# Optimization experiments

Measured on AMD Instinct MI355X. Metric: run time of the kernel, lower is better.

## Reference

```python
import jax, jax.numpy as jnp
import numpy as np

NODE_CARDS = [119, 5, 12, 12, 10, 6, 6, 2, 2]
EDGE_CARDS = [5, 6, 2]
HIDDEN = 256
LAYERS = 5
N = 60000
E = 180000
G = 2048  # num graphs (fixed num_segments)
BN_EPS = 1e-5

_NODE_OFFS = np.concatenate([[0], np.cumsum(NODE_CARDS[:-1])]).astype(np.int32)
_EDGE_OFFS = np.concatenate([[0], np.cumsum(EDGE_CARDS[:-1])]).astype(np.int32)
_NODE_MAX = np.asarray(NODE_CARDS, np.int32) - 1
_EDGE_MAX = np.asarray(EDGE_CARDS, np.int32) - 1


def _cat_sum(x, table, maxs, offs):
    # x: [N, F] int; table: [sum(cards), H] -> [N, H]
    idx = jnp.clip(x, 0, maxs[None, :]) + offs[None, :]
    return table[idx].sum(axis=1)


def setup_inputs() -> dict:
    key = jax.random.key(0)
    ks = jax.random.split(key, 32)
    w = 0.0625  # ~ xavier for 256

    def nrm(k, shape, s=w):
        return jax.random.normal(k, shape, dtype=jnp.float32) * s

    inp = {
        'x': jax.random.randint(ks[0], (N, len(NODE_CARDS)), 0, 119, dtype=jnp.int32),
        'edge_index': jax.random.randint(ks[1], (2, E), 0, N, dtype=jnp.int32),
        'edge_attr': jax.random.randint(ks[2], (E, len(EDGE_CARDS)), 0, 6, dtype=jnp.int32),
        'batch': jnp.sort(jax.random.randint(ks[3], (N,), 0, G, dtype=jnp.int32)),
        # embeddings
        'node_emb': nrm(ks[4], (int(sum(NODE_CARDS)), HIDDEN), 0.1),
        'edge_emb': nrm(ks[5], (int(sum(EDGE_CARDS)), HIDDEN), 0.1),
        'vn_emb': nrm(ks[6], (1, HIDDEN), 0.1),
        # GINE conv: eps + 2-layer MLP per layer (stacked)
        'eps': jnp.zeros((LAYERS,), jnp.float32),
        'W1': nrm(ks[7], (LAYERS, HIDDEN, HIDDEN)),
        'b1': jnp.zeros((LAYERS, HIDDEN), jnp.float32),
        'W2': nrm(ks[8], (LAYERS, HIDDEN, HIDDEN)),
        'b2': jnp.zeros((LAYERS, HIDDEN), jnp.float32),
        # BatchNorm (eval mode: running stats)
        'bn_gamma': jnp.ones((LAYERS, HIDDEN), jnp.float32),
        'bn_beta': jnp.zeros((LAYERS, HIDDEN), jnp.float32),
        'bn_mean': nrm(ks[9], (LAYERS, HIDDEN), 0.02),
        'bn_var': jnp.ones((LAYERS, HIDDEN), jnp.float32),
        # virtual-node MLP per layer
        'vW1': nrm(ks[10], (LAYERS, HIDDEN, HIDDEN)),
        'vb1': jnp.zeros((LAYERS, HIDDEN), jnp.float32),
        'vW2': nrm(ks[11], (LAYERS, HIDDEN, HIDDEN)),
        'vb2': jnp.zeros((LAYERS, HIDDEN), jnp.float32),
        # head MLP (2 layers: hidden->hidden->1)
        'hW1': nrm(ks[12], (HIDDEN, HIDDEN)),
        'hb1': jnp.zeros((HIDDEN,), jnp.float32),
        'hW2': nrm(ks[13], (HIDDEN, 1)),
        'hb2': jnp.zeros((1,), jnp.float32),
    }
    return inp


def reference(x, edge_index, edge_attr, batch,
              node_emb, edge_emb, vn_emb, eps,
              W1, b1, W2, b2,
              bn_gamma, bn_beta, bn_mean, bn_var,
              vW1, vb1, vW2, vb2,
              hW1, hb1, hW2, hb2):
    node_maxs = jnp.asarray(_NODE_MAX)
    node_offs = jnp.asarray(_NODE_OFFS)
    edge_maxs = jnp.asarray(_EDGE_MAX)
    edge_offs = jnp.asarray(_EDGE_OFFS)

    h = _cat_sum(x, node_emb, node_maxs, node_offs)          # [N, H]
    ea = _cat_sum(edge_attr, edge_emb, edge_maxs, edge_offs)  # [E, H]
    src, dst = edge_index[0], edge_index[1]

    vn = jnp.broadcast_to(vn_emb[0], (G, HIDDEN))  # [G, H]

    def mean_pool(h_):
        s = jax.ops.segment_sum(h_, batch, num_segments=G)
        cnt = jax.ops.segment_sum(jnp.ones((h_.shape[0], 1), h_.dtype), batch, num_segments=G)
        return s / jnp.maximum(cnt, 1.0)

    for l in range(LAYERS):
        h = h + vn[batch]
        # GINEConv: msg = relu(x_src + edge_attr); agg scatter-add onto dst
        msg = jax.nn.relu(h[src] + ea)                        # [E, H]
        agg = jax.ops.segment_sum(msg, dst, num_segments=N)   # [N, H]
        z = (1.0 + eps[l]) * h + agg
        z = jax.nn.relu(z @ W1[l] + b1[l]) @ W2[l] + b2[l]
        # BatchNorm1d (eval, running stats)
        z = (z - bn_mean[l]) * (bn_gamma[l] / jnp.sqrt(bn_var[l] + BN_EPS)) + bn_beta[l]
        h = jax.nn.relu(z)
        # virtual-node update
        g = mean_pool(h)
        vn = vn + (jax.nn.relu(g @ vW1[l] + vb1[l]) @ vW2[l] + vb2[l])

    g = mean_pool(h)                                          # [G, H]
    logits = (jax.nn.relu(g @ hW1 + hb1) @ hW2 + hb2).reshape(-1)  # [G]
    return logits
```

## Files before the change

kernel.cpp:

```cpp
#include <hip/hip_runtime.h>

#define NN 60000
#define NE 180000
#define NG 2048
#define NL 5
#define CAP 32

typedef unsigned short u16;
typedef unsigned int u32;
typedef __bf16 bf16x8 __attribute__((ext_vector_type(8)));
typedef float f32x4 __attribute__((ext_vector_type(4)));

__device__ __forceinline__ u16 f2bf(float f) {
    u32 u = __builtin_bit_cast(u32, f);
    u += 0x7FFFu + ((u >> 16) & 1u);
    return (u16)(u >> 16);
}
__device__ __forceinline__ float bf2f(u16 s) {
    return __builtin_bit_cast(float, (u32)s << 16);
}
__device__ __forceinline__ float bflo(u32 w) {
    return __builtin_bit_cast(float, w << 16);
}
__device__ __forceinline__ float bfhi(u32 w) {
    return __builtin_bit_cast(float, w & 0xFFFF0000u);
}
__device__ __forceinline__ u32 pack2bf(float lo, float hi) {
    return (u32)f2bf(lo) | ((u32)f2bf(hi) << 16);
}
__device__ __forceinline__ void gload_lds16(const void* g, void* l) {
    __builtin_amdgcn_global_load_lds(
        (const __attribute__((address_space(1))) unsigned int*)g,
        (__attribute__((address_space(3))) unsigned int*)l, 16, 0, 0);
}
__device__ __forceinline__ int swz(int row, int col) {
    return (row << 9) + ((((col >> 3) ^ (row & 7))) << 4) + ((col & 7) << 1);
}
__device__ __forceinline__ int bswz(int row) {
    return (row & 3) ^ ((row >> 2) & 3);
}

__constant__ int NODE_OFF[9]  = {0, 119, 124, 136, 148, 158, 164, 170, 172};
__constant__ int NODE_MAXC[9] = {118, 4, 11, 11, 9, 5, 5, 1, 1};

__global__ __launch_bounds__(256) void k_prep_weights(
    const float* __restrict__ W1, const float* __restrict__ W2,
    const float* __restrict__ vW1, const float* __restrict__ vW2,
    const float* __restrict__ hW1, u16* __restrict__ Wt)
{
    int mat = blockIdx.x >> 8;
    int n = blockIdx.x & 255;
    int k = threadIdx.x;
    const float* src;
    if (mat < 5)       src = W1 + (size_t)mat * 65536;
    else if (mat < 10) src = W2 + (size_t)(mat - 5) * 65536;
    else if (mat < 15) src = vW1 + (size_t)(mat - 10) * 65536;
    else if (mat < 20) src = vW2 + (size_t)(mat - 15) * 65536;
    else               src = hW1;
    Wt[(size_t)mat * 65536 + n * 256 + k] = f2bf(src[k * 256 + n]);
}

__global__ __launch_bounds__(256) void k_misc(
    const float* __restrict__ eemb, const int* __restrict__ batch,
    const float* __restrict__ vn_emb,
    u16* __restrict__ comb, int* __restrict__ starts,
    float* __restrict__ vn, u16* __restrict__ vnbf, float* __restrict__ gsum)
{
    int b = blockIdx.x;
    if (b < 2048) {
        int i = b * 256 + threadIdx.x;
        float v = vn_emb[i & 255];
        vn[i] = v;
        vnbf[i] = f2bf(v);
        gsum[i] = 0.f;
    } else if (b < 2108) {
        int r = b - 2048, c = threadIdx.x;
        int a0 = r / 12, a1 = (r % 12) / 2, a2 = r & 1;
        comb[r * 256 + c] = f2bf(eemb[a0 * 256 + c] + eemb[(5 + a1) * 256 + c] +
                                 eemb[(11 + a2) * 256 + c]);
    } else {
        int g = (b - 2108) * 256 + threadIdx.x;
        if (g > NG) return;
        int lo = 0, hi = NN;
        while (lo < hi) {
            int mid = (lo + hi) >> 1;
            if (batch[mid] < g) lo = mid + 1; else hi = mid;
        }
        starts[g] = lo;
    }
}

__global__ __launch_bounds__(256) void k_embed(const int* __restrict__ x,
                                               const float* __restrict__ node_emb,
                                               u16* __restrict__ hbf,
                                               int* __restrict__ deg)
{
    int i = blockIdx.x * 4 + (threadIdx.x >> 6);
    if (i >= NN) return;
    if ((threadIdx.x & 63) == 0) deg[i] = 0;
    int c = (threadIdx.x & 63) * 4;
    float4 s = make_float4(0.f, 0.f, 0.f, 0.f);
#pragma unroll
    for (int f = 0; f < 9; ++f) {
        int xv = x[i * 9 + f];
        xv = xv < 0 ? 0 : (xv > NODE_MAXC[f] ? NODE_MAXC[f] : xv);
        const float4 t = *(const float4*)&node_emb[(size_t)(NODE_OFF[f] + xv) * 256 + c];
        s.x += t.x; s.y += t.y; s.z += t.z; s.w += t.w;
    }
    ushort4 o;
    o.x = f2bf(s.x); o.y = f2bf(s.y); o.z = f2bf(s.z); o.w = f2bf(s.w);
    *(ushort4*)&hbf[(size_t)i * 256 + c] = o;
}

__global__ __launch_bounds__(256) void k_bucket(
    const int* __restrict__ src, const int* __restrict__ dst,
    const int* __restrict__ eattr, int* __restrict__ deg, u32* __restrict__ slots)
{
    int e = blockIdx.x * 256 + threadIdx.x;
    if (e >= NE) return;
    int a0 = eattr[e * 3 + 0]; a0 = a0 < 0 ? 0 : (a0 > 4 ? 4 : a0);
    int a1 = eattr[e * 3 + 1]; a1 = a1 < 0 ? 0 : (a1 > 5 ? 5 : a1);
    int a2 = eattr[e * 3 + 2]; a2 = a2 < 0 ? 0 : (a2 > 1 ? 1 : a2);
    u32 code = (u32)(a0 * 12 + a1 * 2 + a2);
    int d = dst[e];
    int p = atomicAdd(&deg[d], 1);
    if (p < CAP) slots[(size_t)d * CAP + p] = (u32)src[e] | (code << 17);
}

__global__ __launch_bounds__(256) void k_agg(
    const u16* __restrict__ hbf, const u16* __restrict__ vnbf,
    const int* __restrict__ batch, const u32* __restrict__ slots,
    const int* __restrict__ deg, const u16* __restrict__ comb,
    u16* __restrict__ Abf, const float* __restrict__ epsp)
{
    const int wid = threadIdx.x >> 6, lane = threadIdx.x & 63;
    const int half = lane >> 5, l32 = lane & 31;
    const int d = blockIdx.x * 8 + wid * 2 + half;
    const int c = l32 * 8;
    int nd = deg[d];
    nd = nd > CAP ? CAP : nd;

    const u32* sl = slots + (size_t)d * CAP;
    u32 sv_l = (l32 < nd) ? sl[l32] : 0u;
    int b_l = (l32 < nd) ? batch[sv_l & 0x1FFFFu] : 0;

    float acc[8] = {0.f, 0.f, 0.f, 0.f, 0.f, 0.f, 0.f, 0.f};
    for (int p = 0; p < nd; ++p) {
        int srcl = (lane & 32) | p;
        u32 sv = (u32)__shfl((int)sv_l, srcl);
        int b  = __shfl(b_l, srcl);
        int s  = (int)(sv & 0x1FFFFu);
        int code = (int)(sv >> 17);
        const uint4 hv = *(const uint4*)&hbf[(size_t)s * 256 + c];
        const uint4 vv = *(const uint4*)&vnbf[(size_t)b * 256 + c];
        const uint4 tv = *(const uint4*)&comb[(size_t)code * 256 + c];
        const u32* hw = (const u32*)&hv;
        const u32* vw = (const u32*)&vv;
        const u32* tw = (const u32*)&tv;
#pragma unroll
        for (int e = 0; e < 4; ++e) {
            acc[e * 2 + 0] += fmaxf(bflo(hw[e]) + bflo(vw[e]) + bflo(tw[e]), 0.f);
            acc[e * 2 + 1] += fmaxf(bfhi(hw[e]) + bfhi(vw[e]) + bfhi(tw[e]), 0.f);
        }
    }

    int bd = batch[d];
    float ep = 1.0f + *epsp;
    const uint4 hd = *(const uint4*)&hbf[(size_t)d * 256 + c];
    const uint4 vd = *(const uint4*)&vnbf[(size_t)bd * 256 + c];
    const u32* hw = (const u32*)&hd;
    const u32* vw = (const u32*)&vd;
    uint4 o;
    u32* op = (u32*)&o;
#pragma unroll
    for (int e = 0; e < 4; ++e) {
        float lo = (bflo(hw[e]) + bflo(vw[e])) * ep + acc[e * 2 + 0];
        float hi = (bfhi(hw[e]) + bfhi(vw[e])) * ep + acc[e * 2 + 1];
        op[e] = pack2bf(lo, hi);
    }
    *(uint4*)&Abf[(size_t)d * 256 + c] = o;
}

__device__ __forceinline__ void stageW32(const u16* __restrict__ W, u16* Bp,
                                         int k0, int tid, int wid)
{
#pragma unroll
    for (int i = 0; i < 2; ++i) {
        int slot = i * 512 + tid;
        int row = slot >> 2, cch = slot & 3;
        int g = cch ^ bswz(row);
        gload_lds16((const char*)W + (size_t)row * 512 + (size_t)k0 * 2 + (g << 4),
                    (char*)Bp + ((i * 512 + wid * 64) << 4));
    }
}

__device__ __forceinline__ void gemmPhase32(const u16* Tl, const u16* Bp,
                                            f32x4 (&acc)[2][4], int p,
                                            int wm, int wn, int cl, int rg)
{
    bf16x8 af[2], bfr[4];
    int ch = p * 4 + rg;
#pragma unroll
    for (int t = 0; t < 2; ++t) {
        int ar = wm + t * 16 + cl;
        af[t] = __builtin_bit_cast(bf16x8,
            *(const uint4*)((const char*)Tl + (ar << 9) + ((ch ^ (ar & 7)) << 4)));
    }
#pragma unroll
    for (int u = 0; u < 4; ++u) {
        int br = wn + u * 16 + cl;
        bfr[u] = __builtin_bit_cast(bf16x8,
            *(const uint4*)((const char*)Bp + (br << 6) + ((rg ^ bswz(br)) << 4)));
    }
#pragma unroll
    for (int t = 0; t < 2; ++t)
#pragma unroll
        for (int u = 0; u < 4; ++u)
            acc[t][u] = __builtin_amdgcn_mfma_f32_16x16x32_bf16(af[t], bfr[u], acc[t][u], 0, 0, 0);
}

__device__ __forceinline__ void writeT(u16* Tl, const f32x4 (&acc)[2][4],
                                       const float* __restrict__ b1,
                                       int wm, int wn, int lane)
{
    const int cl = lane & 15, rg = lane >> 4;
#pragma unroll
    for (int j = 0; j < 4; ++j) {
        int col = wn + j * 16 + cl;
        float bv = b1[col];
#pragma unroll
        for (int i = 0; i < 2; ++i)
#pragma unroll
            for (int r = 0; r < 4; ++r) {
                int row = wm + i * 16 + rg * 4 + r;
                float v = fmaxf(acc[i][j][r] + bv, 0.f);
                *(u16*)((char*)Tl + swz(row, col)) = f2bf(v);
            }
    }
}

__global__ __launch_bounds__(512) void k_mlpP2(
    const u16* __restrict__ Abf, u16* __restrict__ hnxt,
    const int* __restrict__ batch,
    const u16* __restrict__ W1t, const u16* __restrict__ W2t,
    const float* __restrict__ b1, const float* __restrict__ b2,
    const float* __restrict__ bng, const float* __restrict__ bnb,
    const float* __restrict__ bnm, const float* __restrict__ bnv,
    float* __restrict__ gsum)
{
    __shared__ __align__(16) u16 Tl[64 * 256];
    __shared__ __align__(16) u16 Bl[2][256 * 32];
    __shared__ int batchLds[64];
    const int m0 = blockIdx.x * 64;
    const int tid = threadIdx.x, lane = tid & 63, wid = tid >> 6;
    const int wm = (wid >> 2) * 32, wn = (wid & 3) * 64;
    const int cl = lane & 15, rg = lane >> 4;

    if (tid < 64) batchLds[tid] = (m0 + tid < NN) ? batch[m0 + tid] : -1;

#pragma unroll
    for (int i = 0; i < 4; ++i) {
        int slot = i * 512 + tid;
        int row = slot >> 5, cch = slot & 31;
        int g = cch ^ (row & 7);
        gload_lds16((const char*)Abf + (size_t)(m0 + row) * 512 + (g << 4),
                    (char*)Tl + ((i * 512 + wid * 64) << 4));
    }
    stageW32(W1t, Bl[0], 0, tid, wid);
    __syncthreads();

    f32x4 acc1[2][4] = {};
#pragma unroll
    for (int p = 0; p < 8; ++p) {
        if (p < 7) stageW32(W1t, Bl[(p + 1) & 1], (p + 1) * 32, tid, wid);
        else       stageW32(W2t, Bl[0], 0, tid, wid);
        gemmPhase32(Tl, Bl[p & 1], acc1, p, wm, wn, cl, rg);
        __syncthreads();
    }

    writeT(Tl, acc1, b1, wm, wn, lane);
    __syncthreads();

    f32x4 acc2[2][4] = {};
#pragma unroll
    for (int p = 0; p < 8; ++p) {
        if (p < 7) stageW32(W2t, Bl[(p + 1) & 1], (p + 1) * 32, tid, wid);
        gemmPhase32(Tl, Bl[p & 1], acc2, p, wm, wn, cl, rg);
        __syncthreads();
    }

#pragma unroll
    for (int j = 0; j < 4; ++j) {
        int gn = wn + j * 16 + cl;
        float bv = b2[gn];
        float sc = bng[gn] * rsqrtf(bnv[gn] + 1e-5f);
        float sh = bnb[gn] - bnm[gn] * sc;
        float s = 0.f;
        int gcur = -1;
#pragma unroll
        for (int i = 0; i < 2; ++i) {
#pragma unroll
            for (int r = 0; r < 4; ++r) {
                int row = wm + i * 16 + rg * 4 + r;
                int g = batchLds[row];
                float v = acc2[i][j][r] + bv;
                u16 hb = f2bf(fmaxf(v * sc + sh, 0.f));
                if (g >= 0) hnxt[(size_t)(m0 + row) * 256 + gn] = hb;
                if (g != gcur) {
                    if (gcur >= 0) atomicAdd(&gsum[(size_t)gcur * 256 + gn], s);
                    gcur = g; s = 0.f;
                }
                if (g >= 0) s += bf2f(hb);
            }
        }
        if (gcur >= 0) atomicAdd(&gsum[(size_t)gcur * 256 + gn], s);
    }
}

__device__ __forceinline__ void stageW(const u16* __restrict__ W, u16* Bl,
                                       int k0, int tid, int wid)
{
#pragma unroll
    for (int i = 0; i < 4; ++i) {
        int slot = i * 512 + tid;
        int row = slot >> 3, cch = slot & 7;
        int g = cch ^ (row & 7);
        gload_lds16((const char*)W + (size_t)row * 512 + (size_t)k0 * 2 + (g << 4),
                    (char*)Bl + ((i * 512 + wid * 64) << 4));
    }
}

__device__ __forceinline__ void gemm64(const u16* Tl, u16* Bl, const u16* __restrict__ W,
                                       f32x4 (&acc)[2][4], int wm, int wn,
                                       int lane, int tid, int wid)
{
    const int cl = lane & 15;
    for (int k0 = 0; k0 < 256; k0 += 64) {
        __syncthreads();
        stageW(W, Bl, k0, tid, wid);
        __syncthreads();
#pragma unroll
        for (int kw = 0; kw < 2; ++kw) {
            int q = kw * 4 + (lane >> 4);
            int qt = (k0 >> 3) + q;
            bf16x8 af[2], bfr[4];
#pragma unroll
            for (int t = 0; t < 2; ++t) {
                int ar = wm + t * 16 + cl;
                af[t] = __builtin_bit_cast(bf16x8,
                    *(const uint4*)((const char*)Tl + (ar << 9) + ((qt ^ (ar & 7)) << 4)));
            }
#pragma unroll
            for (int t = 0; t < 4; ++t) {
                int br = wn + t * 16 + cl;
                bfr[t] = __builtin_bit_cast(bf16x8,
                    *(const uint4*)((const char*)Bl + (br << 7) + ((q ^ (br & 7)) << 4)));
            }
#pragma unroll
            for (int i = 0; i < 2; ++i)
#pragma unroll
                for (int j = 0; j < 4; ++j)
                    acc[i][j] = __builtin_amdgcn_mfma_f32_16x16x32_bf16(af[i], bfr[j], acc[i][j], 0, 0, 0);
        }
    }
}

__global__ __launch_bounds__(512) void k_vnmlp(
    float* __restrict__ gsum, const int* __restrict__ starts,
    const u16* __restrict__ W1t, const u16* __restrict__ W2t,
    const float* __restrict__ b1, const float* __restrict__ b2,
    float* __restrict__ vn, u16* __restrict__ vnbf)
{
    __shared__ __align__(16) u16 Bl[256 * 64];
    __shared__ __align__(16) u16 Tl[64 * 256];
    const int m0 = blockIdx.x * 64;
    const int tid = threadIdx.x, lane = tid & 63, wid = tid >> 6;
    const int wm = (wid >> 2) * 32, wn = (wid & 3) * 64;
    const int cl = lane & 15, rg = lane >> 4;

    {
        const int c = lane * 4;
#pragma unroll
        for (int n = 0; n < 8; ++n) {
            int row = wid * 8 + n;
            int g = m0 + row;
            float4 sv = *(const float4*)&gsum[(size_t)g * 256 + c];
            *(float4*)&gsum[(size_t)g * 256 + c] = make_float4(0.f, 0.f, 0.f, 0.f);
            float cnt = (float)(starts[g + 1] - starts[g]);
            float inv = 1.0f / fmaxf(cnt, 1.0f);
            ushort4 o;
            o.x = f2bf(sv.x * inv); o.y = f2bf(sv.y * inv);
            o.z = f2bf(sv.z * inv); o.w = f2bf(sv.w * inv);
            *(ushort4*)((char*)Tl + swz(row, c)) = o;
        }
    }
    __syncthreads();

    f32x4 acc1[2][4] = {};
    gemm64(Tl, Bl, W1t, acc1, wm, wn, lane, tid, wid);
    __syncthreads();
    writeT(Tl, acc1, b1, wm, wn, lane);

    f32x4 acc2[2][4] = {};
    gemm64(Tl, Bl, W2t, acc2, wm, wn, lane, tid, wid);

#pragma unroll
    for (int j = 0; j < 4; ++j) {
        int gn = wn + j * 16 + cl;
        float bv = b2[gn];
#pragma unroll
        for (int i = 0; i < 2; ++i) {
#pragma unroll
            for (int r = 0; r < 4; ++r) {
                int gm = m0 + wm + i * 16 + rg * 4 + r;
                size_t idx = (size_t)gm * 256 + gn;
                float nv = vn[idx] + acc2[i][j][r] + bv;
                vn[idx] = nv;
                vnbf[idx] = f2bf(nv);
            }
        }
    }
}

__global__ __launch_bounds__(512) void k_headf(
    const float* __restrict__ gsum, const int* __restrict__ starts,
    const u16* __restrict__ W1t, const float* __restrict__ b1,
    const float* __restrict__ hW2, const float* __restrict__ hb2,
    float* __restrict__ out)
{
    __shared__ __align__(16) u16 Bl[256 * 64];
    __shared__ __align__(16) u16 Tl[64 * 256];
    const int m0 = blockIdx.x * 64;
    const int tid = threadIdx.x, lane = tid & 63, wid = tid >> 6;
    const int wm = (wid >> 2) * 32, wn = (wid & 3) * 64;

    {
        const int c = lane * 4;
#pragma unroll
        for (int n = 0; n < 8; ++n) {
            int row = wid * 8 + n;
            int g = m0 + row;
            float4 sv = *(const float4*)&gsum[(size_t)g * 256 + c];
            float cnt = (float)(starts[g + 1] - starts[g]);
            float inv = 1.0f / fmaxf(cnt, 1.0f);
            ushort4 o;
            o.x = f2bf(sv.x * inv); o.y = f2bf(sv.y * inv);
            o.z = f2bf(sv.z * inv); o.w = f2bf(sv.w * inv);
            *(ushort4*)((char*)Tl + swz(row, c)) = o;
        }
    }
    __syncthreads();

    f32x4 acc1[2][4] = {};
    gemm64(Tl, Bl, W1t, acc1, wm, wn, lane, tid, wid);
    __syncthreads();
    writeT(Tl, acc1, b1, wm, wn, lane);
    __syncthreads();

    int row = tid >> 3, oct = tid & 7;
    float s = 0.f;
#pragma unroll
    for (int c = 0; c < 32; ++c) {
        int col = oct * 32 + c;
        s += bf2f(*(const u16*)((const char*)Tl + swz(row, col))) * hW2[col];
    }
    s += __shfl_down(s, 4);
    s += __shfl_down(s, 2);
    s += __shfl_down(s, 1);
    if (oct == 0) out[m0 + row] = s + hb2[0];
}

extern "C" void kernel_launch(void* const* d_in, const int* in_sizes, int n_in,
                              void* d_out, int out_size, void* d_ws, size_t ws_size,
                              hipStream_t stream)
{
    const int*   x        = (const int*)d_in[0];
    const int*   ei       = (const int*)d_in[1];
    const int*   eattr    = (const int*)d_in[2];
    const int*   batch    = (const int*)d_in[3];
    const float* node_emb = (const float*)d_in[4];
    const float* edge_emb = (const float*)d_in[5];
    const float* vn_emb   = (const float*)d_in[6];
    const float* eps      = (const float*)d_in[7];
    const float* W1       = (const float*)d_in[8];
    const float* b1       = (const float*)d_in[9];
    const float* W2       = (const float*)d_in[10];
    const float* b2       = (const float*)d_in[11];
    const float* bng      = (const float*)d_in[12];
    const float* bnb      = (const float*)d_in[13];
    const float* bnm      = (const float*)d_in[14];
    const float* bnv      = (const float*)d_in[15];
    const float* vW1      = (const float*)d_in[16];
    const float* vb1      = (const float*)d_in[17];
    const float* vW2      = (const float*)d_in[18];
    const float* vb2      = (const float*)d_in[19];
    const float* hW1      = (const float*)d_in[20];
    const float* hb1      = (const float*)d_in[21];
    const float* hW2      = (const float*)d_in[22];
    const float* hb2      = (const float*)d_in[23];
    float* out = (float*)d_out;

    char* ws = (char*)d_ws;
    size_t off = 0;
    auto alloc = [&](size_t b) {
        char* p = ws + off;
        off = (off + b + 255) & ~(size_t)255;
        return p;
    };
    u16*   hbf0 = (u16*)alloc((size_t)NN * 256 * 2);
    u16*   hbf1 = (u16*)alloc((size_t)NN * 256 * 2);
    u16*   Abf  = (u16*)alloc((size_t)NN * 256 * 2 + 65536);
    float* vn   = (float*)alloc((size_t)NG * 256 * 4);
    u16*   vnbf = (u16*)alloc((size_t)NG * 256 * 2);
    float* gsum = (float*)alloc((size_t)NG * 256 * 4);
    u16*   Wt   = (u16*)alloc((size_t)21 * 65536 * 2);
    int*   starts = (int*)alloc((size_t)(NG + 1) * 4);
    u16*   comb = (u16*)alloc((size_t)60 * 256 * 2);
    int*   deg  = (int*)alloc((size_t)NN * 4);
    u32*   slots = (u32*)alloc((size_t)NN * CAP * 4);

    const int* srcI = ei;
    const int* dstI = ei + NE;

    k_prep_weights<<<21 * 256, 256, 0, stream>>>(W1, W2, vW1, vW2, hW1, Wt);
    k_misc<<<2117, 256, 0, stream>>>(edge_emb, batch, vn_emb, comb, starts, vn, vnbf, gsum);
    k_embed<<<NN / 4, 256, 0, stream>>>(x, node_emb, hbf0, deg);
    k_bucket<<<(NE + 255) / 256, 256, 0, stream>>>(srcI, dstI, eattr, deg, slots);

    const int GBIG = (NN + 63) / 64;
    const int GSM  = NG / 64;

    u16* hcur = hbf0;
    u16* hnxt = hbf1;
    for (int l = 0; l < NL; ++l) {
        k_agg<<<NN / 8, 256, 0, stream>>>(hcur, vnbf, batch, slots, deg, comb, Abf, eps + l);
        k_mlpP2<<<GBIG, 512, 0, stream>>>(Abf, hnxt, batch,
                                          Wt + (size_t)(0 + l) * 65536,
                                          Wt + (size_t)(5 + l) * 65536,
                                          b1 + l * 256, b2 + l * 256,
                                          bng + l * 256, bnb + l * 256,
                                          bnm + l * 256, bnv + l * 256,
                                          gsum);
        if (l < NL - 1) {
            k_vnmlp<<<GSM, 512, 0, stream>>>(gsum, starts,
                                             Wt + (size_t)(10 + l) * 65536,
                                             Wt + (size_t)(15 + l) * 65536,
                                             vb1 + l * 256, vb2 + l * 256,
                                             vn, vnbf);
        }
        u16* t = hcur; hcur = hnxt; hnxt = t;
    }
    k_headf<<<GSM, 512, 0, stream>>>(gsum, starts, Wt + (size_t)20 * 65536,
                                     hb1, hW2, hb2, out);
}
```

Measured before the change: 546.2 us.

## Tile weight transpose via LDS, remap agg blocks per XCD, use single-buffer 64-wide GEMM

The weight-prep kernel now transposes 64x64 tiles through shared memory with vectorized loads and stores, replacing strided per-element reads. The aggregation kernel remaps block IDs so that each XCD handles a contiguous range of destination nodes, which is meant to improve L2 locality. The node MLP kernel drops the double-buffered 32-wide K staging and reuses the existing single-buffer 64-wide gemm64 path. That gives fewer barriers per K step but no overlap between staging the weights and the MFMA work.

New measurement: 542.1 us. About the same (-0.8%).

```diff
diff --git a/kernel.cpp b/kernel.cpp
--- a/kernel.cpp
+++ b/kernel.cpp
@@ -36,9 +36,6 @@
 __device__ __forceinline__ int swz(int row, int col) {
     return (row << 9) + ((((col >> 3) ^ (row & 7))) << 4) + ((col & 7) << 1);
 }
-__device__ __forceinline__ int bswz(int row) {
-    return (row & 3) ^ ((row >> 2) & 3);
-}
 
 __constant__ int NODE_OFF[9]  = {0, 119, 124, 136, 148, 158, 164, 170, 172};
 __constant__ int NODE_MAXC[9] = {118, 4, 11, 11, 9, 5, 5, 1, 1};
@@ -48,16 +45,36 @@
     const float* __restrict__ vW1, const float* __restrict__ vW2,
     const float* __restrict__ hW1, u16* __restrict__ Wt)
 {
-    int mat = blockIdx.x >> 8;
-    int n = blockIdx.x & 255;
-    int k = threadIdx.x;
+    __shared__ float lt[64][65];
+    int mat = blockIdx.x >> 4;
+    int tile = blockIdx.x & 15;
+    int tr = (tile >> 2) * 64;
+    int tc = (tile & 3) * 64;
     const float* src;
     if (mat < 5)       src = W1 + (size_t)mat * 65536;
     else if (mat < 10) src = W2 + (size_t)(mat - 5) * 65536;
     else if (mat < 15) src = vW1 + (size_t)(mat - 10) * 65536;
     else if (mat < 20) src = vW2 + (size_t)(mat - 15) * 65536;
     else               src = hW1;
-    Wt[(size_t)mat * 65536 + n * 256 + k] = f2bf(src[k * 256 + n]);
+    int tid = threadIdx.x;
+#pragma unroll
+    for (int r = 0; r < 4; ++r) {
+        int k = (tid >> 4) + r * 16;
+        int c = (tid & 15) * 4;
+        float4 v = *(const float4*)&src[(size_t)(tr + k) * 256 + tc + c];
+        lt[k][c + 0] = v.x; lt[k][c + 1] = v.y;
+        lt[k][c + 2] = v.z; lt[k][c + 3] = v.w;
+    }
+    __syncthreads();
+#pragma unroll
+    for (int r = 0; r < 4; ++r) {
+        int n = (tid >> 4) + r * 16;
+        int k = (tid & 15) * 4;
+        ushort4 o;
+        o.x = f2bf(lt[k + 0][n]); o.y = f2bf(lt[k + 1][n]);
+        o.z = f2bf(lt[k + 2][n]); o.w = f2bf(lt[k + 3][n]);
+        *(ushort4*)&Wt[(size_t)mat * 65536 + (size_t)(tc + n) * 256 + tr + k] = o;
+    }
 }
 
 __global__ __launch_bounds__(256) void k_misc(
@@ -133,9 +150,14 @@
     const int* __restrict__ deg, const u16* __restrict__ comb,
     u16* __restrict__ Abf, const float* __restrict__ epsp)
 {
+    const int nwg = NN / 8;
+    const int q = nwg / 8, r = nwg % 8;
+    int xcd = blockIdx.x % 8, idx = blockIdx.x / 8;
+    int bid = (xcd < r ? xcd * (q + 1) : r * (q + 1) + (xcd - r) * q) + idx;
+
     const int wid = threadIdx.x >> 6, lane = threadIdx.x & 63;
     const int half = lane >> 5, l32 = lane & 31;
-    const int d = blockIdx.x * 8 + wid * 2 + half;
+    const int d = bid * 8 + wid * 2 + half;
     const int c = l32 * 8;
     int nd = deg[d];
     nd = nd > CAP ? CAP : nd;
@@ -181,42 +203,52 @@
     *(uint4*)&Abf[(size_t)d * 256 + c] = o;
 }
 
-__device__ __forceinline__ void stageW32(const u16* __restrict__ W, u16* Bp,
-                                         int k0, int tid, int wid)
-{
-#pragma unroll
-    for (int i = 0; i < 2; ++i) {
+__device__ __forceinline__ void stageW(const u16* __restrict__ W, u16* Bl,
+                                       int k0, int tid, int wid)
+{
+#pragma unroll
+    for (int i = 0; i < 4; ++i) {
         int slot = i * 512 + tid;
-        int row = slot >> 2, cch = slot & 3;
-        int g = cch ^ bswz(row);
+        int row = slot >> 3, cch = slot & 7;
+        int g = cch ^ (row & 7);
         gload_lds16((const char*)W + (size_t)row * 512 + (size_t)k0 * 2 + (g << 4),
-                    (char*)Bp + ((i * 512 + wid * 64) << 4));
-    }
-}
-
-__device__ __forceinline__ void gemmPhase32(const u16* Tl, const u16* Bp,
-                                            f32x4 (&acc)[2][4], int p,
-                                            int wm, int wn, int cl, int rg)
-{
-    bf16x8 af[2], bfr[4];
-    int ch = p * 4 + rg;
-#pragma unroll
-    for (int t = 0; t < 2; ++t) {
-        int ar = wm + t * 16 + cl;
-        af[t] = __builtin_bit_cast(bf16x8,
-            *(const uint4*)((const char*)Tl + (ar << 9) + ((ch ^ (ar & 7)) << 4)));
-    }
-#pragma unroll
-    for (int u = 0; u < 4; ++u) {
-        int br = wn + u * 16 + cl;
-        bfr[u] = __builtin_bit_cast(bf16x8,
-            *(const uint4*)((const char*)Bp + (br << 6) + ((rg ^ bswz(br)) << 4)));
-    }
-#pragma unroll
-    for (int t = 0; t < 2; ++t)
-#pragma unroll
-        for (int u = 0; u < 4; ++u)
-            acc[t][u] = __builtin_amdgcn_mfma_f32_16x16x32_bf16(af[t], bfr[u], acc[t][u], 0, 0, 0);
+                    (char*)Bl + ((i * 512 + wid * 64) << 4));
+    }
+}
+
+__device__ __forceinline__ void gemm64(const u16* Tl, u16* Bl, const u16* __restrict__ W,
+                                       f32x4 (&acc)[2][4], int wm, int wn,
+                                       int lane, int tid, int wid)
+{
+    const int cl = lane & 15;
+    for (int k0 = 0; k0 < 256; k0 += 64) {
+        __syncthreads();
+        stageW(W, Bl, k0, tid, wid);
+        __syncthreads();
+#pragma unroll
+        for (int kw = 0; kw < 2; ++kw) {
+            int q = kw * 4 + (lane >> 4);
+            int qt = (k0 >> 3) + q;
+            bf16x8 af[2], bfr[4];
+#pragma unroll
+            for (int t = 0; t < 2; ++t) {
+                int ar = wm + t * 16 + cl;
+                af[t] = __builtin_bit_cast(bf16x8,
+                    *(const uint4*)((const char*)Tl + (ar << 9) + ((qt ^ (ar & 7)) << 4)));
+            }
+#pragma unroll
+            for (int t = 0; t < 4; ++t) {
+                int br = wn + t * 16 + cl;
+                bfr[t] = __builtin_bit_cast(bf16x8,
+                    *(const uint4*)((const char*)Bl + (br << 7) + ((q ^ (br & 7)) << 4)));
+            }
+#pragma unroll
+            for (int i = 0; i < 2; ++i)
+#pragma unroll
+                for (int j = 0; j < 4; ++j)
+                    acc[i][j] = __builtin_amdgcn_mfma_f32_16x16x32_bf16(af[i], bfr[j], acc[i][j], 0, 0, 0);
+        }
+    }
 }
 
 __device__ __forceinline__ void writeT(u16* Tl, const f32x4 (&acc)[2][4],
@@ -239,7 +271,7 @@
     }
 }
 
-__global__ __launch_bounds__(512) void k_mlpP2(
+__global__ __launch_bounds__(512) void k_mlpP(
     const u16* __restrict__ Abf, u16* __restrict__ hnxt,
     const int* __restrict__ batch,
     const u16* __restrict__ W1t, const u16* __restrict__ W2t,
@@ -248,8 +280,8 @@
     const float* __restrict__ bnm, const float* __restrict__ bnv,
     float* __restrict__ gsum)
 {
+    __shared__ __align__(16) u16 Bl[256 * 64];
     __shared__ __align__(16) u16 Tl[64 * 256];
-    __shared__ __align__(16) u16 Bl[2][256 * 32];
     __shared__ int batchLds[64];
     const int m0 = blockIdx.x * 64;
     const int tid = threadIdx.x, lane = tid & 63, wid = tid >> 6;
@@ -266,28 +298,15 @@
         gload_lds16((const char*)Abf + (size_t)(m0 + row) * 512 + (g << 4),
                     (char*)Tl + ((i * 512 + wid * 64) << 4));
     }
-    stageW32(W1t, Bl[0], 0, tid, wid);
-    __syncthreads();
 
     f32x4 acc1[2][4] = {};
-#pragma unroll
-    for (int p = 0; p < 8; ++p) {
-        if (p < 7) stageW32(W1t, Bl[(p + 1) & 1], (p + 1) * 32, tid, wid);
-        else       stageW32(W2t, Bl[0], 0, tid, wid);
-        gemmPhase32(Tl, Bl[p & 1], acc1, p, wm, wn, cl, rg);
-        __syncthreads();
-    }
-
+    gemm64(Tl, Bl, W1t, acc1, wm, wn, lane, tid, wid);
+    __syncthreads();
     writeT(Tl, acc1, b1, wm, wn, lane);
-    __syncthreads();
 
     f32x4 acc2[2][4] = {};
-#pragma unroll
-    for (int p = 0; p < 8; ++p) {
-        if (p < 7) stageW32(W2t, Bl[(p + 1) & 1], (p + 1) * 32, tid, wid);
-        gemmPhase32(Tl, Bl[p & 1], acc2, p, wm, wn, cl, rg);
-        __syncthreads();
-    }
+    gemm64(Tl, Bl, W2t, acc2, wm, wn, lane, tid, wid);
+    __syncthreads();
 
 #pragma unroll
     for (int j = 0; j < 4; ++j) {
@@ -314,54 +333,6 @@
             }
         }
         if (gcur >= 0) atomicAdd(&gsum[(size_t)gcur * 256 + gn], s);
-    }
-}
-
-__device__ __forceinline__ void stageW(const u16* __restrict__ W, u16* Bl,
-                                       int k0, int tid, int wid)
-{
-#pragma unroll
-    for (int i = 0; i < 4; ++i) {
-        int slot = i * 512 + tid;
-        int row = slot >> 3, cch = slot & 7;
-        int g = cch ^ (row & 7);
-        gload_lds16((const char*)W + (size_t)row * 512 + (size_t)k0 * 2 + (g << 4),
-                    (char*)Bl + ((i * 512 + wid * 64) << 4));
-    }
-}
-
-__device__ __forceinline__ void gemm64(const u16* Tl, u16* Bl, const u16* __restrict__ W,
-                                       f32x4 (&acc)[2][4], int wm, int wn,
-                                       int lane, int tid, int wid)
-{
-    const int cl = lane & 15;
-    for (int k0 = 0; k0 < 256; k0 += 64) {
-        __syncthreads();
-        stageW(W, Bl, k0, tid, wid);
-        __syncthreads();
-#pragma unroll
-        for (int kw = 0; kw < 2; ++kw) {
-            int q = kw * 4 + (lane >> 4);
-            int qt = (k0 >> 3) + q;
-            bf16x8 af[2], bfr[4];
-#pragma unroll
-            for (int t = 0; t < 2; ++t) {
-                int ar = wm + t * 16 + cl;
-                af[t] = __builtin_bit_cast(bf16x8,
-                    *(const uint4*)((const char*)Tl + (ar << 9) + ((qt ^ (ar & 7)) << 4)));
-            }
-#pragma unroll
-            for (int t = 0; t < 4; ++t) {
-                int br = wn + t * 16 + cl;
-                bfr[t] = __builtin_bit_cast(bf16x8,
-                    *(const uint4*)((const char*)Bl + (br << 7) + ((q ^ (br & 7)) << 4)));
-            }
-#pragma unroll
-            for (int i = 0; i < 2; ++i)
-#pragma unroll
-                for (int j = 0; j < 4; ++j)
-                    acc[i][j] = __builtin_amdgcn_mfma_f32_16x16x32_bf16(af[i], bfr[j], acc[i][j], 0, 0, 0);
-        }
     }
 }
 
@@ -522,7 +493,7 @@
     const int* srcI = ei;
     const int* dstI = ei + NE;
 
-    k_prep_weights<<<21 * 256, 256, 0, stream>>>(W1, W2, vW1, vW2, hW1, Wt);
+    k_prep_weights<<<21 * 16, 256, 0, stream>>>(W1, W2, vW1, vW2, hW1, Wt);
     k_misc<<<2117, 256, 0, stream>>>(edge_emb, batch, vn_emb, comb, starts, vn, vnbf, gsum);
     k_embed<<<NN / 4, 256, 0, stream>>>(x, node_emb, hbf0, deg);
     k_bucket<<<(NE + 255) / 256, 256, 0, stream>>>(srcI, dstI, eattr, deg, slots);
@@ -534,13 +505,13 @@
     u16* hnxt = hbf1;
     for (int l = 0; l < NL; ++l) {
         k_agg<<<NN / 8, 256, 0, stream>>>(hcur, vnbf, batch, slots, deg, comb, Abf, eps + l);
-        k_mlpP2<<<GBIG, 512, 0, stream>>>(Abf, hnxt, batch,
-                                          Wt + (size_t)(0 + l) * 65536,
-                                          Wt + (size_t)(5 + l) * 65536,
-                                          b1 + l * 256, b2 + l * 256,
-                                          bng + l * 256, bnb + l * 256,
-                                          bnm + l * 256, bnv + l * 256,
-                                          gsum);
+        k_mlpP<<<GBIG, 512, 0, stream>>>(Abf, hnxt, batch,
+                                         Wt + (size_t)(0 + l) * 65536,
+                                         Wt + (size_t)(5 + l) * 65536,
+                                         b1 + l * 256, b2 + l * 256,
+                                         bng + l * 256, bnb + l * 256,
+                                         bnm + l * 256, bnv + l * 256,
+                                         gsum);
         if (l < NL - 1) {
             k_vnmlp<<<GSM, 512, 0, stream>>>(gsum, starts,
                                              Wt + (size_t)(10 + l) * 65536,
```
